# Kernel optimization log

Measured on AMD Instinct MI355X. Metric: run time of the kernel, lower is better.

## Reference

```python
import jax, jax.numpy as jnp
import numpy as np


def _dw_conv(x, w, ks):
    # x: [1, B*k, H, W], w: [B*k, 1, ks, ks], groups = B*k depthwise conv
    pad = (ks - 1) // 2
    return jax.lax.conv_general_dilated(
        x, w, window_strides=(1, 1), padding=[(pad, pad), (pad, pad)],
        feature_group_count=x.shape[1],
        dimension_numbers=('NCHW', 'OIHW', 'NCHW'))


def setup_inputs() -> dict:
    key = jax.random.key(0)
    ks = jax.random.split(key, 12)
    B, Cin, M, O, H, W = 8, 256, 256, 256, 128, 128
    k = 128  # static top-k channel count (eval-mode: ceil(M * clamp(mean(scores),0.25,1.0)) ~ M/2)
    inp = {
        'x': jax.random.normal(ks[0], (B, Cin, H, W), jnp.float32),
        'pw1_w': jax.random.normal(ks[1], (M, Cin), jnp.float32) * 0.02,
        'pw1_b': jnp.zeros((M,), jnp.float32),
        'fc1_w': jax.random.normal(ks[2], (2 * M, M), jnp.float32) * 0.02,
        'fc1_b': jnp.zeros((2 * M,), jnp.float32),
        'fc2_w': jax.random.normal(ks[3], (M, 2 * M), jnp.float32) * 0.02,
        'fc2_b': jnp.zeros((M,), jnp.float32),
        'off_w': jax.random.normal(ks[4], (6, M), jnp.float32) * 0.02,
        'off_b': jnp.zeros((6,), jnp.float32),
        'dw3': jax.random.normal(ks[5], (M, 1, 3, 3), jnp.float32) * 0.1,
        'dw5': jax.random.normal(ks[6], (M, 1, 5, 5), jnp.float32) * 0.1,
        'dw7': jax.random.normal(ks[7], (M, 1, 7, 7), jnp.float32) * 0.1,
        'pw_w': jax.random.normal(ks[8], (O, 3 * M), jnp.float32) * 0.02,
        'pw_b': jnp.zeros((O,), jnp.float32),
        'k': k,
    }
    return inp


def reference(x, pw1_w, pw1_b, fc1_w, fc1_b, fc2_w, fc2_b, off_w, off_b,
              dw3, dw5, dw7, pw_w, pw_b, k):
    B, _, H, W = x.shape
    residual = x  # identity shortcut (stride=1, in==out)
    # pointwise_1 (1x1 conv)
    h = jnp.einsum('bchw,oc->bohw', x, pw1_w) + pw1_b[None, :, None, None]
    # WidthPredictor (eval mode): scores from GAP of pre-ReLU features
    gap = h.mean(axis=(2, 3))                                   # [B, M]
    hid = jax.nn.relu(gap @ fc1_w.T + fc1_b)
    scores = jax.nn.sigmoid(hid @ fc2_w.T + fc2_b)              # [B, M]
    _, idx = jax.lax.top_k(scores, k)                           # [B, k]
    mask = jnp.zeros_like(scores).at[jnp.arange(B)[:, None], idx].set(1.0)
    h = jax.nn.relu(h)
    # offset generator: GAP -> 1x1 conv -> tanh
    gap2 = h.mean(axis=(2, 3))
    offsets = jnp.tanh(gap2 @ off_w.T + off_b).reshape(B, 3, 2)  # [B, branches, 2]
    # mask then take first k channels (as in original: (x*mask)[:, :k])
    sel = (h * mask[:, :, None, None])[:, :k]                    # [B, k, H, W]
    conv_in = sel.reshape(1, B * k, H, W)
    outs = []
    for i, (ksz, base) in enumerate([(3, dw3), (5, dw5), (7, dw7)]):
        scale = jax.nn.sigmoid(offsets[:, i, 0]).reshape(B, 1, 1, 1, 1)
        shift = jnp.tanh(offsets[:, i, 1]).reshape(B, 1, 1, 1, 1)
        w = base[:k][None] * (1.0 + scale) + shift               # [B, k, 1, ks, ks]
        y = _dw_conv(conv_in, w.reshape(B * k, 1, ksz, ksz), ksz)
        outs.append(y.reshape(B, k, H, W))
    fused = jnp.concatenate(outs, axis=1)                        # [B, 3k, H, W]
    sel_pw = pw_w[:, :3 * k]                                     # [O, 3k]
    out = jnp.einsum('bchw,oc->bohw', fused, sel_pw) + pw_b[None, :, None, None]
    return out + residual
```

## Files before the change

### kernel.cpp

```cpp
#include <hip/hip_runtime.h>
#include <math.h>

constexpr int B  = 8;
constexpr int C  = 256;
constexpr int M  = 256;
constexpr int O  = 256;
constexpr int H  = 128;
constexpr int W  = 128;
constexpr int HW = H * W;
constexpr int K  = 128;

using f16   = _Float16;
using f16x2 = __attribute__((ext_vector_type(2))) _Float16;
using f16x8 = __attribute__((ext_vector_type(8))) _Float16;
using f32x4 = __attribute__((ext_vector_type(4))) float;

constexpr size_t WS_MEANX = 0;
constexpr size_t WS_MASK  = 2048;
constexpr size_t WS_G2    = 4096;
constexpr size_t WS_OFF   = 6144;
constexpr size_t WS_WE3   = 6208;
constexpr size_t WS_WE5   = 15424;
constexpr size_t WS_WE7   = 41024;
constexpr size_t WS_WT1G  = 91200;
constexpr size_t WS_WT2G  = 123968;
constexpr size_t WS_SELH  = 173120;
constexpr size_t WS_BIG   = 8561728;

__global__ __launch_bounds__(256) void kT(const float* __restrict__ pw1_w,
                                          const float* __restrict__ pw_w,
                                          const float* __restrict__ fc1_w,
                                          const float* __restrict__ fc2_w,
                                          float* __restrict__ ws) {
  f16* wt1g = (f16*)(ws + WS_WT1G);
  f16* wt2g = (f16*)(ws + WS_WT2G);
  int t = blockIdx.x * 256 + threadIdx.x;
  if (t < 65536) {
    int ks = t >> 13, fr = (t >> 9) & 15, l = (t >> 3) & 63, j = t & 7;
    int o = fr * 16 + (l & 15);
    int c = ks * 32 + ((l >> 4) << 3) + j;
    wt1g[t] = (f16)pw1_w[o * C + c];
  }
  if (t < 98304) {
    int ks = t >> 13, fr = (t >> 9) & 15, l = (t >> 3) & 63, j = t & 7;
    int o = fr * 16 + (l & 15);
    int cc = ks * 32 + ((l >> 4) << 3) + j;
    wt2g[t] = (f16)pw_w[(size_t)o * 768 + cc];
  }
  if (t < 2048) {
    ws[WS_MEANX + t] = 0.f;
    ws[WS_G2 + t]    = 0.f;
  }
  if (t < 32768) {
    float4 a = ((const float4*)fc1_w)[t];
    float4 c = ((const float4*)fc2_w)[t];
    float dead = a.x + a.y + a.z + a.w + c.x + c.y + c.z + c.w;
    asm volatile("" :: "v"(dead));
  }
}

__global__ __launch_bounds__(256) void kAT(const float* __restrict__ x,
                                           float* __restrict__ ws) {
  float* meanx = ws + WS_MEANX;
  f16* xh      = (f16*)(ws + WS_BIG);
  int b = blockIdx.z, ko = blockIdx.y, p0 = blockIdx.x * 256;
  __shared__ float sx[8][256];
  int t = threadIdx.x;
  int c8 = t >> 5, pg = t & 31;
  const float* xp = x + (size_t)(b * 256 + ko * 8 + c8) * HW + p0 + pg * 8;
  float4 v0 = ((const float4*)xp)[0];
  float4 v1 = ((const float4*)xp)[1];
  *(float4*)&sx[c8][pg * 8]     = v0;
  *(float4*)&sx[c8][pg * 8 + 4] = v1;
  float s = v0.x + v0.y + v0.z + v0.w + v1.x + v1.y + v1.z + v1.w;
#pragma unroll
  for (int off = 16; off > 0; off >>= 1) s += __shfl_xor(s, off, 32);
  if (pg == 0) atomicAdd(&meanx[b * 256 + ko * 8 + c8], s * (1.f / HW));
  __syncthreads();
  f16x8 o;
#pragma unroll
  for (int j = 0; j < 8; j++) o[j] = (f16)sx[j][t];
  *(f16x8*)&xh[((size_t)(b * 32 + ko) * HW + p0 + t) * 8] = o;
}

__global__ __launch_bounds__(256) void kB(const float* __restrict__ pw1_w,
                                          const float* __restrict__ pw1_b,
                                          const float* __restrict__ fc1_w,
                                          const float* __restrict__ fc1_b,
                                          const float* __restrict__ fc2_w,
                                          const float* __restrict__ fc2_b,
                                          float* __restrict__ ws) {
  int b = blockIdx.x;
  const float* meanx = ws + WS_MEANX + b * C;
  float* maskg = ws + WS_MASK;
  __shared__ float s_gap[M];
  __shared__ float s_hid[512];
  __shared__ float s_sc[M];
  int t = threadIdx.x;
  int lane = t & 63, wv = t >> 6;

  float4 mx = ((const float4*)meanx)[lane];
  for (int o0 = wv * 64; o0 < wv * 64 + 64; o0 += 4) {
    float s[4];
#pragma unroll
    for (int j = 0; j < 4; j++) {
      float4 w = ((const float4*)(pw1_w + (size_t)(o0 + j) * C))[lane];
      s[j] = mx.x * w.x + mx.y * w.y + mx.z * w.z + mx.w * w.w;
    }
#pragma unroll
    for (int off = 32; off > 0; off >>= 1)
#pragma unroll
      for (int j = 0; j < 4; j++) s[j] += __shfl_xor(s[j], off, 64);
    if (lane == 0) {
#pragma unroll
      for (int j = 0; j < 4; j++) s_gap[o0 + j] = s[j] + pw1_b[o0 + j];
    }
  }
  __syncthreads();

  float4 g4 = ((const float4*)s_gap)[lane];
  for (int j0 = wv * 128; j0 < wv * 128 + 128; j0 += 4) {
    float s[4];
#pragma unroll
    for (int j = 0; j < 4; j++) {
      float4 w = ((const float4*)(fc1_w + (size_t)(j0 + j) * M))[lane];
      s[j] = g4.x * w.x + g4.y * w.y + g4.z * w.z + g4.w * w.w;
    }
#pragma unroll
    for (int off = 32; off > 0; off >>= 1)
#pragma unroll
      for (int j = 0; j < 4; j++) s[j] += __shfl_xor(s[j], off, 64);
    if (lane == 0) {
#pragma unroll
      for (int j = 0; j < 4; j++) {
        float v = s[j] + fc1_b[j0 + j];
        s_hid[j0 + j] = v > 0.f ? v : 0.f;
      }
    }
  }
  __syncthreads();

  float4 h0 = ((const float4*)s_hid)[lane];
  float4 h1 = ((const float4*)s_hid)[lane + 64];
  for (int o0 = wv * 64; o0 < wv * 64 + 64; o0 += 4) {
    float s[4];
#pragma unroll
    for (int j = 0; j < 4; j++) {
      const float4* wr = (const float4*)(fc2_w + (size_t)(o0 + j) * 512);
      float4 w0 = wr[lane];
      float4 w1 = wr[lane + 64];
      s[j] = h0.x * w0.x + h0.y * w0.y + h0.z * w0.z + h0.w * w0.w +
             h1.x * w1.x + h1.y * w1.y + h1.z * w1.z + h1.w * w1.w;
    }
#pragma unroll
    for (int off = 32; off > 0; off >>= 1)
#pragma unroll
      for (int j = 0; j < 4; j++) s[j] += __shfl_xor(s[j], off, 64);
    if (lane == 0) {
#pragma unroll
      for (int j = 0; j < 4; j++) {
        float v = s[j] + fc2_b[o0 + j];
        s_sc[o0 + j] = 1.f / (1.f + expf(-v));
      }
    }
  }
  __syncthreads();

  {
    int j = t;
    float sj = s_sc[j];
    int cnt = 0;
    for (int m = 0; m < M; m++) {
      float sm = s_sc[m];
      cnt += (sm > sj) || (sm == sj && m < j);
    }
    maskg[b * M + j] = (cnt < K) ? 1.f : 0.f;
  }
}

__global__ __launch_bounds__(256) void kCm(const float* __restrict__ pw1_b,
                                           float* __restrict__ ws) {
  const f16* wt1g = (const f16*)(ws + WS_WT1G);
  const f16* xh   = (const f16*)(ws + WS_BIG);
  float* gap2sum  = ws + WS_G2;
  f16* selh       = (f16*)(ws + WS_SELH);
  int b  = blockIdx.z;
  int p0 = blockIdx.x * 64;

  int t = threadIdx.x, l = t & 63, w = t >> 6;
  int q = l >> 4, n = l & 15;

  const f16* bbase = xh + (size_t)(b * 32 + q) * (HW * 8) + (size_t)(p0 + n) * 8;
  const f16* abase = wt1g + (size_t)(w * 4) * 512 + (size_t)l * 8;

#define LDA1(dst, ks)                                                          \
  _Pragma("unroll") for (int mt = 0; mt < 4; mt++)                             \
      dst[mt] = *(const f16x8*)(abase + (size_t)((ks) * 16 + mt) * 512);
#define LDB1(dst, ks)                                                          \
  _Pragma("unroll") for (int nt = 0; nt < 4; nt++)                             \
      dst[nt] = *(const f16x8*)(bbase + (size_t)(ks) * (4 * HW * 8) + nt * 128);
#define STEP1(af, bf)                                                          \
  _Pragma("unroll") for (int mt = 0; mt < 4; mt++)                             \
      _Pragma("unroll") for (int nt = 0; nt < 4; nt++)                         \
          acc[mt][nt] = __builtin_amdgcn_mfma_f32_16x16x32_f16(                \
              af[mt], bf[nt], acc[mt][nt], 0, 0, 0);

  f16x8 bA[4], bB[4], aT[4];
  LDB1(bA, 0)

  f32x4 acc[4][4];
#pragma unroll
  for (int mt = 0; mt < 4; mt++) {
    int obase = w * 64 + mt * 16 + q * 4;
#pragma unroll
    for (int nt = 0; nt < 4; nt++)
#pragma unroll
      for (int r = 0; r < 4; r++) acc[mt][nt][r] = pw1_b[obase + r];
  }

#pragma unroll
  for (int ks = 0; ks < 8; ks += 2) {
    if (ks + 1 < 8) LDB1(bB, ks + 1)
    LDA1(aT, ks)
    STEP1(aT, bA)
    if (ks + 2 < 8) LDB1(bA, ks + 2)
    if (ks + 1 < 8) { LDA1(aT, ks + 1) STEP1(aT, bB) }
  }
#undef LDA1
#undef LDB1
#undef STEP1

#pragma unroll
  for (int mt = 0; mt < 4; mt++) {
    float rsum[4] = {0.f, 0.f, 0.f, 0.f};
    int obase = w * 64 + mt * 16 + q * 4;
#pragma unroll
    for (int nt = 0; nt < 4; nt++) {
      int p = p0 + nt * 16 + n;
#pragma unroll
      for (int r = 0; r < 4; r++) {
        float h = acc[mt][nt][r];
        h = h > 0.f ? h : 0.f;
        rsum[r] += h;
        int o = obase + r;
        if (o < K) selh[((size_t)(b * K + o)) * HW + p] = (f16)h;
      }
    }
#pragma unroll
    for (int off = 1; off < 16; off <<= 1)
#pragma unroll
      for (int r = 0; r < 4; r++) rsum[r] += __shfl_xor(rsum[r], off, 64);
    if (n == 0) {
#pragma unroll
      for (int r = 0; r < 4; r++)
        atomicAdd(&gap2sum[b * M + obase + r], rsum[r]);
    }
  }
}

__global__ __launch_bounds__(256) void kD1(const float* __restrict__ off_w,
                                           const float* __restrict__ off_b,
                                           float* __restrict__ ws) {
  const float* gap2sum = ws + WS_G2;
  float* offv = ws + WS_OFF;
  __shared__ float s_off[48];
  int t = threadIdx.x;
  int lane = t & 63, wv = t >> 6;
  for (int id = wv; id < 48; id += 4) {
    int b = id / 6, j = id % 6;
    float4 g = ((const float4*)(gap2sum + b * M))[lane];
    float4 w = ((const float4*)(off_w + (size_t)j * M))[lane];
    float s = (g.x * w.x + g.y * w.y + g.z * w.z + g.w * w.w) * (1.f / HW);
#pragma unroll
    for (int off = 32; off > 0; off >>= 1) s += __shfl_xor(s, off, 64);
    if (lane == 0) s_off[id] = tanhf(s + off_b[j]);
  }
  __syncthreads();
  if (t < 24) {
    int b = t / 3, i = t % 3;
    offv[t]      = 1.f + 1.f / (1.f + expf(-s_off[b * 6 + 2 * i]));
    offv[24 + t] = tanhf(s_off[b * 6 + 2 * i + 1]);
  }
}

__global__ __launch_bounds__(256) void kD2(const float* __restrict__ dw3,
                                           const float* __restrict__ dw5,
                                           const float* __restrict__ dw7,
                                           float* __restrict__ ws) {
  const float* offv  = ws + WS_OFF;
  const float* maskg = ws + WS_MASK;
  float* wE3 = ws + WS_WE3;
  float* wE5 = ws + WS_WE5;
  float* wE7 = ws + WS_WE7;
  int tid = blockIdx.x * 256 + threadIdx.x;
  int stride = gridDim.x * 256;
  for (int i = tid; i < B * K * 9; i += stride) {
    int b = i / (K * 9), rem = i % (K * 9), c = rem / 9;
    wE3[i] = (dw3[rem] * offv[b * 3 + 0] + offv[24 + b * 3 + 0]) * maskg[b * M + c];
  }
  for (int i = tid; i < B * K * 25; i += stride) {
    int b = i / (K * 25), rem = i % (K * 25), c = rem / 25;
    wE5[i] = (dw5[rem] * offv[b * 3 + 1] + offv[24 + b * 3 + 1]) * maskg[b * M + c];
  }
  for (int i = tid; i < B * K * 49; i += stride) {
    int b = i / (K * 49), rem = i % (K * 49), c = rem / 49;
    wE7[i] = (dw7[rem] * offv[b * 3 + 2] + offv[24 + b * 3 + 2]) * maskg[b * M + c];
  }
}

__global__ __launch_bounds__(256) void kEm(const float* __restrict__ ws_ro,
                                           float* __restrict__ ws) {
  constexpr int SP = 1768;
  __shared__ f16 sm[8 * SP];
  const f16* selh = (const f16*)(ws_ro + WS_SELH);
  f16* yh2        = (f16*)(ws + WS_BIG);
  int bx = blockIdx.x;
  int slab = bx >> 1, chalf = bx & 1;
  int ko = blockIdx.y, b = blockIdx.z;
  int r0 = slab * 16, c0 = chalf * 64;

  for (int i = threadIdx.x; i < 8 * 220; i += 256) {
    int chn = i / 220, rem = i - chn * 220;
    int rr = rem / 10, chunk = rem - rr * 10;
    int gy = r0 - 3 + rr, g0 = c0 - 8 + chunk * 8;
    f16x8 v = {};
    if (gy >= 0 && gy < H && g0 >= 0 && g0 < W)
      v = *(const f16x8*)&selh[(size_t)(b * 128 + ko * 8 + chn) * HW + gy * W + g0];
    *(f16x8*)&sm[chn * SP + rr * 80 + chunk * 8] = v;
  }
  __syncthreads();

  int t = threadIdx.x;
  int ch = t & 7, cp = t >> 3;
  int cglob = c0 + cp * 2;

#define CONV_BRANCH(KS, BR, WSOFF, NW, SOFF)                                   \
  {                                                                            \
    constexpr int P = (KS - 1) / 2;                                            \
    const float* wp = ws_ro + WSOFF + (size_t)(b * 128 + ko * 8 + ch) * (KS*KS); \
    float w[KS * KS];                                                          \
    _Pragma("unroll") for (int i = 0; i < KS * KS; i++) w[i] = wp[i];          \
    float a0[16], a1[16];                                                      \
    _Pragma("unroll") for (int r = 0; r < 16; r++) { a0[r] = 0.f; a1[r] = 0.f; } \
    _Pragma("unroll") for (int iy = 0; iy < 16 + 2 * P; iy++) {                \
      int hr = iy + (3 - P);                                                   \
      const f16x2* rowp = (const f16x2*)(sm + ch * SP + hr * 80);              \
      float vv[2 * NW];                                                        \
      _Pragma("unroll") for (int u = 0; u < NW; u++) {                         \
        f16x2 pr = rowp[cp + SOFF + u];                                        \
        vv[2 * u]     = (float)pr[0];                                          \
        vv[2 * u + 1] = (float)pr[1];                                          \
      }                                                                        \
      _Pragma("unroll") for (int rr = 0; rr < 16; rr++) {                      \
        int dy = iy - rr;                                                      \
        if (dy >= 0 && dy < KS) {                                              \
          _Pragma("unroll") for (int dx = 0; dx < KS; dx++) {                  \
            int m = (8 - P) + dx - 2 * SOFF;                                   \
            a0[rr] += vv[m]     * w[dy * KS + dx];                             \
            a1[rr] += vv[m + 1] * w[dy * KS + dx];                             \
          }                                                                    \
        }                                                                      \
      }                                                                        \
    }                                                                          \
    f16* op = yh2 + (size_t)(b * 48 + BR * 16 + ko) * HW * 8;                  \
    _Pragma("unroll") for (int rr = 0; rr < 16; rr++) {                        \
      size_t pa = ((size_t)(r0 + rr) * W + cglob) * 8 + ch;                    \
      op[pa]     = (f16)a0[rr];                                                \
      op[pa + 8] = (f16)a1[rr];                                                \
    }                                                                          \
  }

  CONV_BRANCH(3, 0, WS_WE3, 3, 3)
  CONV_BRANCH(5, 1, WS_WE5, 3, 3)
  CONV_BRANCH(7, 2, WS_WE7, 5, 2)
#undef CONV_BRANCH
}

__global__ __launch_bounds__(256) void kFm(const float* __restrict__ x,
                                           const float* __restrict__ pw_b,
                                           const float* __restrict__ ws,
                                           float* __restrict__ out) {
  const f16* wt2g = (const f16*)(ws + WS_WT2G);
  const f16* yh2  = (const f16*)(ws + WS_BIG);
  int b  = blockIdx.z;
  int p0 = blockIdx.x * 64;

  int t = threadIdx.x, l = t & 63, w = t >> 6;
  int q = l >> 4, n = l & 15;

  const f16* bbase = yh2 + (size_t)(b * 48 + q) * (HW * 8) + (size_t)(p0 + n) * 8;
  const f16* abase = wt2g + (size_t)(w * 4) * 512 + (size_t)l * 8;

#define LDA2(dst, ks)                                                          \
  _Pragma("unroll") for (int mt = 0; mt < 4; mt++)                             \
      dst[mt] = *(const f16x8*)(abase + (size_t)((ks) * 16 + mt) * 512);
#define LDB2(dst, ks)                                                          \
  _Pragma("unroll") for (int nt = 0; nt < 4; nt++)                             \
      dst[nt] = *(const f16x8*)(bbase + (size_t)(ks) * (4 * HW * 8) + nt * 128);
#define STEP2(af, bf)                                                          \
  _Pragma("unroll") for (int mt = 0; mt < 4; mt++)                             \
      _Pragma("unroll") for (int nt = 0; nt < 4; nt++)                         \
          acc[mt][nt] = __builtin_amdgcn_mfma_f32_16x16x32_f16(                \
              af[mt], bf[nt], acc[mt][nt], 0, 0, 0);

  f16x8 bA[4], bB[4], aT[4];
  LDB2(bA, 0)

  f32x4 acc[4][4];
#pragma unroll
  for (int mt = 0; mt < 4; mt++) {
    int obase = w * 64 + mt * 16 + q * 4;
    float b4[4];
#pragma unroll
    for (int r = 0; r < 4; r++) b4[r] = pw_b[obase + r];
#pragma unroll
    for (int nt = 0; nt < 4; nt++) {
      int p = p0 + nt * 16 + n;
#pragma unroll
      for (int r = 0; r < 4; r++) {
        size_t idx = ((size_t)b * O + obase + r) * HW + p;
        acc[mt][nt][r] = b4[r] + __builtin_nontemporal_load(&x[idx]);
      }
    }
  }

#pragma unroll
  for (int ks = 0; ks < 12; ks += 2) {
    if (ks + 1 < 12) LDB2(bB, ks + 1)
    LDA2(aT, ks)
    STEP2(aT, bA)
    if (ks + 2 < 12) LDB2(bA, ks + 2)
    if (ks + 1 < 12) { LDA2(aT, ks + 1) STEP2(aT, bB) }
  }
#undef LDA2
#undef LDB2
#undef STEP2

#pragma unroll
  for (int mt = 0; mt < 4; mt++) {
    int obase = w * 64 + mt * 16 + q * 4;
#pragma unroll
    for (int nt = 0; nt < 4; nt++) {
      int p = p0 + nt * 16 + n;
#pragma unroll
      for (int r = 0; r < 4; r++) {
        size_t idx = ((size_t)b * O + obase + r) * HW + p;
        out[idx] = acc[mt][nt][r];
      }
    }
  }
}

extern "C" void kernel_launch(void* const* d_in, const int* in_sizes, int n_in,
                              void* d_out, int out_size, void* d_ws, size_t ws_size,
                              hipStream_t stream) {
  const float* x     = (const float*)d_in[0];
  const float* pw1_w = (const float*)d_in[1];
  const float* pw1_b = (const float*)d_in[2];
  const float* fc1_w = (const float*)d_in[3];
  const float* fc1_b = (const float*)d_in[4];
  const float* fc2_w = (const float*)d_in[5];
  const float* fc2_b = (const float*)d_in[6];
  const float* off_w = (const float*)d_in[7];
  const float* off_b = (const float*)d_in[8];
  const float* dw3   = (const float*)d_in[9];
  const float* dw5   = (const float*)d_in[10];
  const float* dw7   = (const float*)d_in[11];
  const float* pw_w  = (const float*)d_in[12];
  const float* pw_b  = (const float*)d_in[13];
  float* out = (float*)d_out;
  float* ws  = (float*)d_ws;

  kT<<<384, 256, 0, stream>>>(pw1_w, pw_w, fc1_w, fc2_w, ws);
  kAT<<<dim3(HW / 256, 32, B), 256, 0, stream>>>(x, ws);
  kB<<<B, 256, 0, stream>>>(pw1_w, pw1_b, fc1_w, fc1_b, fc2_w, fc2_b, ws);
  kCm<<<dim3(HW / 64, 1, B), 256, 0, stream>>>(pw1_b, ws);
  kD1<<<1, 256, 0, stream>>>(off_w, off_b, ws);
  kD2<<<84, 256, 0, stream>>>(dw3, dw5, dw7, ws);
  kEm<<<dim3(16, 16, B), 256, 0, stream>>>(ws, ws);
  kFm<<<dim3(HW / 64, 1, B), 256, 0, stream>>>(x, pw_b, ws, out);
}
```

Baseline: 551.8 us.

## Stage activation tile in shared memory for both 1x1-conv MFMA GEMMs

In the two pointwise GEMM kernels, each block now loads its whole activation tile (32 or 48 channel groups × 64 pixels, f16) into LDS once with coalesced loads. The four waves then read it from LDS instead of each wave re-reading the same data from global memory, and the weight loads are double-buffered in registers instead. This cuts redundant global/L2 traffic for the B operand, since all four waves share identical B fragments. The cost is 32–48 KB of LDS per block, which may limit occupancy, plus a block barrier before compute.

```diff
diff --git a/kernel.cpp b/kernel.cpp
--- a/kernel.cpp
+++ b/kernel.cpp
@@ -184,50 +184,63 @@
   const f16* xh   = (const f16*)(ws + WS_BIG);
   float* gap2sum  = ws + WS_G2;
   f16* selh       = (f16*)(ws + WS_SELH);
+  __shared__ f16 Bs[32 * 512];
   int b  = blockIdx.z;
   int p0 = blockIdx.x * 64;
 
   int t = threadIdx.x, l = t & 63, w = t >> 6;
   int q = l >> 4, n = l & 15;
 
-  const f16* bbase = xh + (size_t)(b * 32 + q) * (HW * 8) + (size_t)(p0 + n) * 8;
+  {
+    f16x8 tmp[8];
+#pragma unroll
+    for (int i = 0; i < 8; i++) {
+      int s = t + i * 256;
+      int ko = s >> 6, ll = s & 63;
+      tmp[i] = *(const f16x8*)&xh[((size_t)(b * 32 + ko) * HW + p0 + ll) * 8];
+    }
+#pragma unroll
+    for (int i = 0; i < 8; i++)
+      *(f16x8*)&Bs[(size_t)(t + i * 256) * 8] = tmp[i];
+  }
+
+  f32x4 acc[4][4];
+#pragma unroll
+  for (int mt = 0; mt < 4; mt++) {
+    int obase = w * 64 + mt * 16 + q * 4;
+#pragma unroll
+    for (int nt = 0; nt < 4; nt++)
+#pragma unroll
+      for (int r = 0; r < 4; r++) acc[mt][nt][r] = pw1_b[obase + r];
+  }
+  __syncthreads();
+
   const f16* abase = wt1g + (size_t)(w * 4) * 512 + (size_t)l * 8;
 
 #define LDA1(dst, ks)                                                          \
   _Pragma("unroll") for (int mt = 0; mt < 4; mt++)                             \
       dst[mt] = *(const f16x8*)(abase + (size_t)((ks) * 16 + mt) * 512);
-#define LDB1(dst, ks)                                                          \
+#define LDBS1(dst, ks)                                                         \
   _Pragma("unroll") for (int nt = 0; nt < 4; nt++)                             \
-      dst[nt] = *(const f16x8*)(bbase + (size_t)(ks) * (4 * HW * 8) + nt * 128);
+      dst[nt] = *(const f16x8*)&Bs[(size_t)(((ks) * 4 + q) * 64 + nt * 16 + n) * 8];
 #define STEP1(af, bf)                                                          \
   _Pragma("unroll") for (int mt = 0; mt < 4; mt++)                             \
       _Pragma("unroll") for (int nt = 0; nt < 4; nt++)                         \
           acc[mt][nt] = __builtin_amdgcn_mfma_f32_16x16x32_f16(                \
               af[mt], bf[nt], acc[mt][nt], 0, 0, 0);
 
-  f16x8 bA[4], bB[4], aT[4];
-  LDB1(bA, 0)
-
-  f32x4 acc[4][4];
-#pragma unroll
-  for (int mt = 0; mt < 4; mt++) {
-    int obase = w * 64 + mt * 16 + q * 4;
-#pragma unroll
-    for (int nt = 0; nt < 4; nt++)
-#pragma unroll
-      for (int r = 0; r < 4; r++) acc[mt][nt][r] = pw1_b[obase + r];
-  }
-
+  f16x8 aA[4], aB[4], bC[4], bD[4];
+  LDA1(aA, 0)
 #pragma unroll
   for (int ks = 0; ks < 8; ks += 2) {
-    if (ks + 1 < 8) LDB1(bB, ks + 1)
-    LDA1(aT, ks)
-    STEP1(aT, bA)
-    if (ks + 2 < 8) LDB1(bA, ks + 2)
-    if (ks + 1 < 8) { LDA1(aT, ks + 1) STEP1(aT, bB) }
+    if (ks + 1 < 8) LDA1(aB, ks + 1)
+    LDBS1(bC, ks)
+    STEP1(aA, bC)
+    if (ks + 2 < 8) LDA1(aA, ks + 2)
+    if (ks + 1 < 8) { LDBS1(bD, ks + 1) STEP1(aB, bD) }
   }
 #undef LDA1
-#undef LDB1
+#undef LDBS1
 #undef STEP1
 
 #pragma unroll
@@ -382,58 +395,71 @@
                                            float* __restrict__ out) {
   const f16* wt2g = (const f16*)(ws + WS_WT2G);
   const f16* yh2  = (const f16*)(ws + WS_BIG);
+  __shared__ f16 Bs[48 * 512];
   int b  = blockIdx.z;
   int p0 = blockIdx.x * 64;
 
   int t = threadIdx.x, l = t & 63, w = t >> 6;
   int q = l >> 4, n = l & 15;
 
-  const f16* bbase = yh2 + (size_t)(b * 48 + q) * (HW * 8) + (size_t)(p0 + n) * 8;
+  {
+    f16x8 tmp[12];
+#pragma unroll
+    for (int i = 0; i < 12; i++) {
+      int s = t + i * 256;
+      int ko = s >> 6, ll = s & 63;
+      tmp[i] = *(const f16x8*)&yh2[((size_t)(b * 48 + ko) * HW + p0 + ll) * 8];
+    }
+#pragma unroll
+    for (int i = 0; i < 12; i++)
+      *(f16x8*)&Bs[(size_t)(t + i * 256) * 8] = tmp[i];
+  }
+
+  f32x4 acc[4][4];
+#pragma unroll
+  for (int mt = 0; mt < 4; mt++) {
+    int obase = w * 64 + mt * 16 + q * 4;
+    float b4[4];
+#pragma unroll
+    for (int r = 0; r < 4; r++) b4[r] = pw_b[obase + r];
+#pragma unroll
+    for (int nt = 0; nt < 4; nt++) {
+      int p = p0 + nt * 16 + n;
+#pragma unroll
+      for (int r = 0; r < 4; r++) {
+        size_t idx = ((size_t)b * O + obase + r) * HW + p;
+        acc[mt][nt][r] = b4[r] + __builtin_nontemporal_load(&x[idx]);
+      }
+    }
+  }
+  __syncthreads();
+
   const f16* abase = wt2g + (size_t)(w * 4) * 512 + (size_t)l * 8;
 
 #define LDA2(dst, ks)                                                          \
   _Pragma("unroll") for (int mt = 0; mt < 4; mt++)                             \
       dst[mt] = *(const f16x8*)(abase + (size_t)((ks) * 16 + mt) * 512);
-#define LDB2(dst, ks)                                                          \
+#define LDBS2(dst, ks)                                                         \
   _Pragma("unroll") for (int nt = 0; nt < 4; nt++)                             \
-      dst[nt] = *(const f16x8*)(bbase + (size_t)(ks) * (4 * HW * 8) + nt * 128);
+      dst[nt] = *(const f16x8*)&Bs[(size_t)(((ks) * 4 + q) * 64 + nt * 16 + n) * 8];
 #define STEP2(af, bf)                                                          \
   _Pragma("unroll") for (int mt = 0; mt < 4; mt++)                             \
       _Pragma("unroll") for (int nt = 0; nt < 4; nt++)                         \
           acc[mt][nt] = __builtin_amdgcn_mfma_f32_16x16x32_f16(                \
               af[mt], bf[nt], acc[mt][nt], 0, 0, 0);
 
-  f16x8 bA[4], bB[4], aT[4];
-  LDB2(bA, 0)
-
-  f32x4 acc[4][4];
-#pragma unroll
-  for (int mt = 0; mt < 4; mt++) {
-    int obase = w * 64 + mt * 16 + q * 4;
-    float b4[4];
-#pragma unroll
-    for (int r = 0; r < 4; r++) b4[r] = pw_b[obase + r];
-#pragma unroll
-    for (int nt = 0; nt < 4; nt++) {
-      int p = p0 + nt * 16 + n;
-#pragma unroll
-      for (int r = 0; r < 4; r++) {
-        size_t idx = ((size_t)b * O + obase + r) * HW + p;
-        acc[mt][nt][r] = b4[r] + __builtin_nontemporal_load(&x[idx]);
-      }
-    }
-  }
-
+  f16x8 aA[4], aB[4], bC[4], bD[4];
+  LDA2(aA, 0)
 #pragma unroll
   for (int ks = 0; ks < 12; ks += 2) {
-    if (ks + 1 < 12) LDB2(bB, ks + 1)
-    LDA2(aT, ks)
-    STEP2(aT, bA)
-    if (ks + 2 < 12) LDB2(bA, ks + 2)
-    if (ks + 1 < 12) { LDA2(aT, ks + 1) STEP2(aT, bB) }
+    if (ks + 1 < 12) LDA2(aB, ks + 1)
+    LDBS2(bC, ks)
+    STEP2(aA, bC)
+    if (ks + 2 < 12) LDA2(aA, ks + 2)
+    if (ks + 1 < 12) { LDBS2(bD, ks + 1) STEP2(aB, bD) }
   }
 #undef LDA2
-#undef LDB2
+#undef LDBS2
 #undef STEP2
 
 #pragma unroll
```

After: 558.1 us. About the same (+1.1%).
